# Kernel optimization log

Measured on AMD Instinct MI355X. Metric: run time of the kernel, lower is better.

The kernel has to match this reference:

```python
import jax, jax.numpy as jnp
import numpy as np

N_VISIBLE = 4096
N_HIDDEN = 4096
BATCH = 8192


def setup_inputs() -> dict:
    key = jax.random.key(0)
    k_x, k_w = jax.random.split(key)
    input_data = jax.random.uniform(k_x, (BATCH, N_VISIBLE), dtype=jnp.float32)
    # xavier_uniform with sigmoid gain (=1.0): limit = sqrt(6/(fan_in+fan_out))
    limit = float(np.sqrt(6.0 / (N_VISIBLE + N_HIDDEN)))
    W = jax.random.uniform(k_w, (N_VISIBLE, N_HIDDEN), dtype=jnp.float32,
                           minval=-limit, maxval=limit)
    hidden_bias = jnp.zeros((N_HIDDEN,), dtype=jnp.float32)
    return {"input_data": input_data, "W": W, "hidden_bias": hidden_bias}


def reference(input_data, W, hidden_bias):
    # RBM.sample_hidden_2 (forward): sigmoid(x @ W + b), batched over samples.
    # (The torch code loops per sample with host syncs; same math, vectorized.)
    hid_prob = jax.nn.sigmoid(jnp.matmul(input_data, W) + hidden_bias)
    return hid_prob
```

## Files before the change

kernel.cpp:

```cpp
#include <hip/hip_runtime.h>
#include <cstdint>

#define MDIM 8192
#define NDIM 4096
#define KDIM 4096

typedef __bf16 bf16x8 __attribute__((ext_vector_type(8)));
typedef float f32x4 __attribute__((ext_vector_type(4)));

__device__ __forceinline__ void gload_lds16(const void* g, void* l) {
    __builtin_amdgcn_global_load_lds(
        (const __attribute__((address_space(1))) uint32_t*)g,
        (__attribute__((address_space(3))) uint32_t*)l, 16, 0, 0);
}

__device__ __forceinline__ unsigned short bf16_bits(float f) {
    __bf16 b = (__bf16)f;
    return __builtin_bit_cast(unsigned short, b);
}

__device__ __forceinline__ int detect_f32(const void* X) {
    int ok = 1;
    if (threadIdx.x < 128) {
        unsigned short h = ((const unsigned short*)X)[threadIdx.x];
        ok = (h <= 0x3F80);
    }
    return __syncthreads_and(ok) ? 0 : 1;
}

__global__ __launch_bounds__(256) void cvt_x(const float* __restrict__ X,
                                             __bf16* __restrict__ Xb) {
    const int f32 = detect_f32(X);
    if (!f32) return;
    const long base = ((long)blockIdx.x * 256 + threadIdx.x) * 16;
#pragma unroll
    for (int c = 0; c < 2; ++c) {
        float4 v0 = *(const float4*)(X + base + c * 8);
        float4 v1 = *(const float4*)(X + base + c * 8 + 4);
        unsigned short r[8] = {bf16_bits(v0.x), bf16_bits(v0.y), bf16_bits(v0.z),
                               bf16_bits(v0.w), bf16_bits(v1.x), bf16_bits(v1.y),
                               bf16_bits(v1.z), bf16_bits(v1.w)};
        *(uint4*)(Xb + base + c * 8) = *(const uint4*)r;
    }
}

__global__ __launch_bounds__(256) void transpose_w(const void* __restrict__ X,
                                                   const void* __restrict__ W,
                                                   __bf16* __restrict__ WT) {
    __shared__ unsigned short tile[64 * 65];
    const int f32 = detect_f32(X);
    const int t = threadIdx.x;
    const int k0 = blockIdx.y * 64;
    const int n0 = blockIdx.x * 64;
    if (f32) {
        const float* Wf = (const float*)W;
#pragma unroll
        for (int p = 0; p < 4; ++p) {
            const int ch = p * 256 + t;
            const int kr = ch >> 4;
            const int nc = ch & 15;
            float4 v = *(const float4*)(Wf + (long)(k0 + kr) * NDIM + n0 + nc * 4);
            tile[(nc * 4 + 0) * 65 + kr] = bf16_bits(v.x);
            tile[(nc * 4 + 1) * 65 + kr] = bf16_bits(v.y);
            tile[(nc * 4 + 2) * 65 + kr] = bf16_bits(v.z);
            tile[(nc * 4 + 3) * 65 + kr] = bf16_bits(v.w);
        }
    } else {
        const __bf16* Wb = (const __bf16*)W;
#pragma unroll
        for (int p = 0; p < 2; ++p) {
            const int ch = p * 256 + t;
            const int kr = ch >> 3;
            const int nc = ch & 7;
            uint4 v = *(const uint4*)(Wb + (long)(k0 + kr) * NDIM + n0 + nc * 8);
            const unsigned short* e = (const unsigned short*)&v;
#pragma unroll
            for (int i = 0; i < 8; ++i) tile[(nc * 8 + i) * 65 + kr] = e[i];
        }
    }
    __syncthreads();
#pragma unroll
    for (int p = 0; p < 2; ++p) {
        const int ch = p * 256 + t;
        const int nr = ch >> 3;
        const int kc = ch & 7;
        unsigned short r[8];
#pragma unroll
        for (int i = 0; i < 8; ++i) r[i] = tile[nr * 65 + kc * 8 + i];
        *(uint4*)(WT + (long)(n0 + nr) * KDIM + k0 + kc * 8) = *(uint4*)r;
    }
}

template <int MODE>
__global__ __launch_bounds__(256) void gemm_bias_sigmoid(
    const void* __restrict__ X, const __bf16* __restrict__ Xb,
    const void* __restrict__ Wp, const __bf16* __restrict__ WT,
    const void* __restrict__ bias, void* __restrict__ out) {
    __shared__ __bf16 sA[128 * 32];
    __shared__ __bf16 sB[128 * 32];
    const int f32 = detect_f32(X);
    const int t = threadIdx.x;
    const int lane = t & 63;
    const int wid = t >> 6;
    const int m0 = blockIdx.y * 128;
    const int n0 = blockIdx.x * 128;
    const int wm = (wid & 1) * 64;
    const int wn = (wid >> 1) * 64;
    const int lrow = lane & 15;
    const int quad = lane >> 4;

    f32x4 acc[4][4] = {};

    const int srow = t >> 2;
    const int schk = t & 3;
    __bf16* ldsA = sA + wid * 512;
    __bf16* ldsB = sB + wid * 512;

    const int arow = t >> 1;
    const int acol = (t & 1) * 16;
    const int fp = t & 15;
    const int fc = t >> 4;
    uint32_t* sB32 = (uint32_t*)sB;

    auto compute = [&]() {
        bf16x8 aF[4], bF[4];
        const __bf16* pa = sA + (wm + lrow) * 32 + quad * 8;
        const __bf16* pb = sB + (wn + lrow) * 32 + quad * 8;
#pragma unroll
        for (int i = 0; i < 4; ++i) aF[i] = *(const bf16x8*)(pa + i * 512);
#pragma unroll
        for (int j = 0; j < 4; ++j) bF[j] = *(const bf16x8*)(pb + j * 512);
#pragma unroll
        for (int i = 0; i < 4; ++i)
#pragma unroll
            for (int j = 0; j < 4; ++j)
                acc[i][j] = __builtin_amdgcn_mfma_f32_16x16x32_bf16(
                    aF[i], bF[j], acc[i][j], 0, 0, 0);
    };

    if (MODE <= 1 && !(MODE == 1 && f32)) {
        const __bf16* Abf = (MODE == 0 && f32) ? Xb : (const __bf16*)X;
        const __bf16* gA = Abf + (long)(m0 + srow) * KDIM + schk * 8;
        const __bf16* gB = WT + (long)(n0 + srow) * KDIM + schk * 8;
        for (int kt = 0; kt < KDIM / 32; ++kt) {
            const __bf16* a0 = gA + kt * 32;
            gload_lds16(a0, ldsA);
            gload_lds16(a0 + (long)64 * KDIM, ldsA + 2048);
            const __bf16* b0 = gB + kt * 32;
            gload_lds16(b0, ldsB);
            gload_lds16(b0 + (long)64 * KDIM, ldsB + 2048);
            __syncthreads();
            compute();
            __syncthreads();
        }
    } else if (MODE == 1) {
        const float* Xf = (const float*)X;
        const __bf16* gB = WT + (long)(n0 + srow) * KDIM + schk * 8;
        for (int kt = 0; kt < KDIM / 32; ++kt) {
            const __bf16* b0 = gB + kt * 32;
            gload_lds16(b0, ldsB);
            gload_lds16(b0 + (long)64 * KDIM, ldsB + 2048);
            const float* ap = Xf + (long)(m0 + arow) * KDIM + kt * 32 + acol;
            float4 v0 = *(const float4*)(ap);
            float4 v1 = *(const float4*)(ap + 4);
            float4 v2 = *(const float4*)(ap + 8);
            float4 v3 = *(const float4*)(ap + 12);
            unsigned short r[16] = {
                bf16_bits(v0.x), bf16_bits(v0.y), bf16_bits(v0.z), bf16_bits(v0.w),
                bf16_bits(v1.x), bf16_bits(v1.y), bf16_bits(v1.z), bf16_bits(v1.w),
                bf16_bits(v2.x), bf16_bits(v2.y), bf16_bits(v2.z), bf16_bits(v2.w),
                bf16_bits(v3.x), bf16_bits(v3.y), bf16_bits(v3.z), bf16_bits(v3.w)};
            *(uint4*)(sA + arow * 32 + acol) = *(const uint4*)(r);
            *(uint4*)(sA + arow * 32 + acol + 8) = *(const uint4*)(r + 8);
            __syncthreads();
            compute();
            __syncthreads();
        }
    } else {
        if (!f32) {
            const __bf16* gA = (const __bf16*)X + (long)(m0 + srow) * KDIM + schk * 8;
            const __bf16* Wb = (const __bf16*)Wp;
            for (int kt = 0; kt < KDIM / 32; ++kt) {
                const __bf16* a0 = gA + kt * 32;
                gload_lds16(a0, ldsA);
                gload_lds16(a0 + (long)64 * KDIM, ldsA + 2048);
                const __bf16* w0 = Wb + (long)(kt * 32 + 2 * fp) * NDIM + n0 + fc * 8;
                uint4 g0 = *(const uint4*)(w0);
                uint4 g1 = *(const uint4*)(w0 + NDIM);
                const unsigned short* e0 = (const unsigned short*)&g0;
                const unsigned short* e1 = (const unsigned short*)&g1;
#pragma unroll
                for (int i = 0; i < 8; ++i)
                    sB32[(fc * 8 + i) * 16 + fp] =
                        (uint32_t)e0[i] | ((uint32_t)e1[i] << 16);
                __syncthreads();
                compute();
                __syncthreads();
            }
        } else {
            const float* Xf = (const float*)X;
            const float* Wf = (const float*)Wp;
            for (int kt = 0; kt < KDIM / 32; ++kt) {
                const float* ap = Xf + (long)(m0 + arow) * KDIM + kt * 32 + acol;
                float4 v0 = *(const float4*)(ap);
                float4 v1 = *(const float4*)(ap + 4);
                float4 v2 = *(const float4*)(ap + 8);
                float4 v3 = *(const float4*)(ap + 12);
                unsigned short r[16] = {
                    bf16_bits(v0.x), bf16_bits(v0.y), bf16_bits(v0.z), bf16_bits(v0.w),
                    bf16_bits(v1.x), bf16_bits(v1.y), bf16_bits(v1.z), bf16_bits(v1.w),
                    bf16_bits(v2.x), bf16_bits(v2.y), bf16_bits(v2.z), bf16_bits(v2.w),
                    bf16_bits(v3.x), bf16_bits(v3.y), bf16_bits(v3.z), bf16_bits(v3.w)};
                *(uint4*)(sA + arow * 32 + acol) = *(const uint4*)(r);
                *(uint4*)(sA + arow * 32 + acol + 8) = *(const uint4*)(r + 8);
                const float* w0 = Wf + (long)(kt * 32 + 2 * fp) * NDIM + n0 + fc * 8;
                float4 u0 = *(const float4*)(w0);
                float4 u1 = *(const float4*)(w0 + 4);
                float4 u2 = *(const float4*)(w0 + NDIM);
                float4 u3 = *(const float4*)(w0 + NDIM + 4);
                float k0v[8] = {u0.x, u0.y, u0.z, u0.w, u1.x, u1.y, u1.z, u1.w};
                float k1v[8] = {u2.x, u2.y, u2.z, u2.w, u3.x, u3.y, u3.z, u3.w};
#pragma unroll
                for (int i = 0; i < 8; ++i)
                    sB32[(fc * 8 + i) * 16 + fp] =
                        (uint32_t)bf16_bits(k0v[i]) |
                        ((uint32_t)bf16_bits(k1v[i]) << 16);
                __syncthreads();
                compute();
                __syncthreads();
            }
        }
    }

    const int crow = m0 + wm + quad * 4;
    if (f32) {
        float* of = (float*)out;
        const float* bf = (const float*)bias;
#pragma unroll
        for (int j = 0; j < 4; ++j) {
            const int col = n0 + wn + j * 16 + lrow;
            const float bv = bf[col];
#pragma unroll
            for (int i = 0; i < 4; ++i) {
                const long rbase = (long)(crow + i * 16) * NDIM + col;
#pragma unroll
                for (int r = 0; r < 4; ++r) {
                    const float x = acc[i][j][r] + bv;
                    of[rbase + (long)r * NDIM] = 1.0f / (1.0f + __expf(-x));
                }
            }
        }
    } else {
        __bf16* ob = (__bf16*)out;
        const __bf16* bb = (const __bf16*)bias;
#pragma unroll
        for (int j = 0; j < 4; ++j) {
            const int col = n0 + wn + j * 16 + lrow;
            const float bv = (float)bb[col];
#pragma unroll
            for (int i = 0; i < 4; ++i) {
                const long rbase = (long)(crow + i * 16) * NDIM + col;
#pragma unroll
                for (int r = 0; r < 4; ++r) {
                    const float x = acc[i][j][r] + bv;
                    ob[rbase + (long)r * NDIM] = (__bf16)(1.0f / (1.0f + __expf(-x)));
                }
            }
        }
    }
}

extern "C" void kernel_launch(void* const* d_in, const int* in_sizes, int n_in,
                              void* d_out, int out_size, void* d_ws,
                              size_t ws_size, hipStream_t stream) {
    const void* X = d_in[0];
    const void* W = d_in[1];
    const void* bias = d_in[2];

    const size_t wt_bytes = (size_t)KDIM * NDIM * sizeof(__bf16);
    const size_t xb_bytes = (size_t)MDIM * KDIM * sizeof(__bf16);
    dim3 gg(NDIM / 128, MDIM / 128);

    if (ws_size >= wt_bytes + xb_bytes) {
        __bf16* WT = (__bf16*)d_ws;
        __bf16* Xb = (__bf16*)((char*)d_ws + wt_bytes);
        cvt_x<<<MDIM * KDIM / (256 * 16), 256, 0, stream>>>((const float*)X, Xb);
        transpose_w<<<dim3(NDIM / 64, KDIM / 64), 256, 0, stream>>>(X, W, WT);
        gemm_bias_sigmoid<0><<<gg, 256, 0, stream>>>(X, Xb, W, WT, bias, d_out);
    } else if (ws_size >= wt_bytes) {
        __bf16* WT = (__bf16*)d_ws;
        transpose_w<<<dim3(NDIM / 64, KDIM / 64), 256, 0, stream>>>(X, W, WT);
        gemm_bias_sigmoid<1><<<gg, 256, 0, stream>>>(X, nullptr, W, WT, bias, d_out);
    } else {
        gemm_bias_sigmoid<2><<<gg, 256, 0, stream>>>(X, nullptr, W, nullptr, bias, d_out);
    }
}
```

Baseline: 628.2 us.

## Merge prep kernels into one launch and double GEMM K-tile to 64

Folds the X conversion and W transpose into a single prep kernel launch, indexed by block id, to save one launch. In MODE 0 the main GEMM now stages 64-wide K tiles (twice the LDS), so each barrier pair covers two MFMA sub-steps and the number of synchronisations halves. The cost is more LDS per block, which may lower occupancy. The LDS rows stay unswizzled at a 128-byte stride, so fragment reads may hit bank conflicts.

```diff
diff --git a/kernel.cpp b/kernel.cpp
--- a/kernel.cpp
+++ b/kernel.cpp
@@ -28,19 +28,68 @@
     return __syncthreads_and(ok) ? 0 : 1;
 }
 
-__global__ __launch_bounds__(256) void cvt_x(const float* __restrict__ X,
-                                             __bf16* __restrict__ Xb) {
+__global__ __launch_bounds__(256) void prep(const void* __restrict__ X,
+                                            const void* __restrict__ W,
+                                            __bf16* __restrict__ Xb,
+                                            __bf16* __restrict__ WT) {
     const int f32 = detect_f32(X);
-    if (!f32) return;
-    const long base = ((long)blockIdx.x * 256 + threadIdx.x) * 16;
-#pragma unroll
-    for (int c = 0; c < 2; ++c) {
-        float4 v0 = *(const float4*)(X + base + c * 8);
-        float4 v1 = *(const float4*)(X + base + c * 8 + 4);
-        unsigned short r[8] = {bf16_bits(v0.x), bf16_bits(v0.y), bf16_bits(v0.z),
-                               bf16_bits(v0.w), bf16_bits(v1.x), bf16_bits(v1.y),
-                               bf16_bits(v1.z), bf16_bits(v1.w)};
-        *(uint4*)(Xb + base + c * 8) = *(const uint4*)r;
+    const int t = threadIdx.x;
+    if (blockIdx.x < 8192) {
+        if (!f32) return;
+        const float* Xf = (const float*)X;
+        const long base = ((long)blockIdx.x * 256 + t) * 16;
+#pragma unroll
+        for (int c = 0; c < 2; ++c) {
+            float4 v0 = *(const float4*)(Xf + base + c * 8);
+            float4 v1 = *(const float4*)(Xf + base + c * 8 + 4);
+            unsigned short r[8] = {bf16_bits(v0.x), bf16_bits(v0.y),
+                                   bf16_bits(v0.z), bf16_bits(v0.w),
+                                   bf16_bits(v1.x), bf16_bits(v1.y),
+                                   bf16_bits(v1.z), bf16_bits(v1.w)};
+            *(uint4*)(Xb + base + c * 8) = *(const uint4*)r;
+        }
+        return;
+    }
+    __shared__ unsigned short tile[64 * 65];
+    const int bid = blockIdx.x - 8192;
+    const int n0 = (bid & 63) * 64;
+    const int k0 = (bid >> 6) * 64;
+    if (f32) {
+        const float* Wf = (const float*)W;
+#pragma unroll
+        for (int p = 0; p < 4; ++p) {
+            const int ch = p * 256 + t;
+            const int kr = ch >> 4;
+            const int nc = ch & 15;
+            float4 v = *(const float4*)(Wf + (long)(k0 + kr) * NDIM + n0 + nc * 4);
+            tile[(nc * 4 + 0) * 65 + kr] = bf16_bits(v.x);
+            tile[(nc * 4 + 1) * 65 + kr] = bf16_bits(v.y);
+            tile[(nc * 4 + 2) * 65 + kr] = bf16_bits(v.z);
+            tile[(nc * 4 + 3) * 65 + kr] = bf16_bits(v.w);
+        }
+    } else {
+        const __bf16* Wb = (const __bf16*)W;
+#pragma unroll
+        for (int p = 0; p < 2; ++p) {
+            const int ch = p * 256 + t;
+            const int kr = ch >> 3;
+            const int nc = ch & 7;
+            uint4 v = *(const uint4*)(Wb + (long)(k0 + kr) * NDIM + n0 + nc * 8);
+            const unsigned short* e = (const unsigned short*)&v;
+#pragma unroll
+            for (int i = 0; i < 8; ++i) tile[(nc * 8 + i) * 65 + kr] = e[i];
+        }
+    }
+    __syncthreads();
+#pragma unroll
+    for (int p = 0; p < 2; ++p) {
+        const int ch = p * 256 + t;
+        const int nr = ch >> 3;
+        const int kc = ch & 7;
+        unsigned short r[8];
+#pragma unroll
+        for (int i = 0; i < 8; ++i) r[i] = tile[nr * 65 + kc * 8 + i];
+        *(uint4*)(WT + (long)(n0 + nr) * KDIM + k0 + kc * 8) = *(uint4*)r;
     }
 }
 
@@ -96,8 +145,8 @@
     const void* __restrict__ X, const __bf16* __restrict__ Xb,
     const void* __restrict__ Wp, const __bf16* __restrict__ WT,
     const void* __restrict__ bias, void* __restrict__ out) {
-    __shared__ __bf16 sA[128 * 32];
-    __shared__ __bf16 sB[128 * 32];
+    __shared__ __bf16 sA[128 * 64];
+    __shared__ __bf16 sB[128 * 64];
     const int f32 = detect_f32(X);
     const int t = threadIdx.x;
     const int lane = t & 63;
@@ -111,73 +160,108 @@
 
     f32x4 acc[4][4] = {};
 
-    const int srow = t >> 2;
-    const int schk = t & 3;
-    __bf16* ldsA = sA + wid * 512;
-    __bf16* ldsB = sB + wid * 512;
-
-    const int arow = t >> 1;
-    const int acol = (t & 1) * 16;
-    const int fp = t & 15;
-    const int fc = t >> 4;
-    uint32_t* sB32 = (uint32_t*)sB;
-
-    auto compute = [&]() {
-        bf16x8 aF[4], bF[4];
-        const __bf16* pa = sA + (wm + lrow) * 32 + quad * 8;
-        const __bf16* pb = sB + (wn + lrow) * 32 + quad * 8;
-#pragma unroll
-        for (int i = 0; i < 4; ++i) aF[i] = *(const bf16x8*)(pa + i * 512);
-#pragma unroll
-        for (int j = 0; j < 4; ++j) bF[j] = *(const bf16x8*)(pb + j * 512);
-#pragma unroll
-        for (int i = 0; i < 4; ++i)
-#pragma unroll
-            for (int j = 0; j < 4; ++j)
-                acc[i][j] = __builtin_amdgcn_mfma_f32_16x16x32_bf16(
-                    aF[i], bF[j], acc[i][j], 0, 0, 0);
-    };
-
-    if (MODE <= 1 && !(MODE == 1 && f32)) {
-        const __bf16* Abf = (MODE == 0 && f32) ? Xb : (const __bf16*)X;
-        const __bf16* gA = Abf + (long)(m0 + srow) * KDIM + schk * 8;
-        const __bf16* gB = WT + (long)(n0 + srow) * KDIM + schk * 8;
-        for (int kt = 0; kt < KDIM / 32; ++kt) {
-            const __bf16* a0 = gA + kt * 32;
-            gload_lds16(a0, ldsA);
-            gload_lds16(a0 + (long)64 * KDIM, ldsA + 2048);
-            const __bf16* b0 = gB + kt * 32;
-            gload_lds16(b0, ldsB);
-            gload_lds16(b0 + (long)64 * KDIM, ldsB + 2048);
+    if constexpr (MODE == 0) {
+        const __bf16* Abf = f32 ? Xb : (const __bf16*)X;
+        const int r8 = lane >> 3;
+        const int c8 = lane & 7;
+        const __bf16* gA = Abf + (long)(m0 + wid * 32 + r8) * KDIM + c8 * 8;
+        const __bf16* gB = WT + (long)(n0 + wid * 32 + r8) * KDIM + c8 * 8;
+        __bf16* lA = sA + wid * 32 * 64;
+        __bf16* lB = sB + wid * 32 * 64;
+
+        for (int kt = 0; kt < KDIM / 64; ++kt) {
+            const int kb = kt * 64;
+#pragma unroll
+            for (int i = 0; i < 4; ++i) {
+                gload_lds16(gA + kb + (long)i * 8 * KDIM, lA + i * 512);
+                gload_lds16(gB + kb + (long)i * 8 * KDIM, lB + i * 512);
+            }
             __syncthreads();
-            compute();
+#pragma unroll
+            for (int h = 0; h < 2; ++h) {
+                bf16x8 aF[4], bF[4];
+                const __bf16* pa = sA + (wm + lrow) * 64 + h * 32 + quad * 8;
+                const __bf16* pb = sB + (wn + lrow) * 64 + h * 32 + quad * 8;
+#pragma unroll
+                for (int i = 0; i < 4; ++i)
+                    aF[i] = *(const bf16x8*)(pa + i * 1024);
+#pragma unroll
+                for (int j = 0; j < 4; ++j)
+                    bF[j] = *(const bf16x8*)(pb + j * 1024);
+#pragma unroll
+                for (int i = 0; i < 4; ++i)
+#pragma unroll
+                    for (int j = 0; j < 4; ++j)
+                        acc[i][j] = __builtin_amdgcn_mfma_f32_16x16x32_bf16(
+                            aF[i], bF[j], acc[i][j], 0, 0, 0);
+            }
             __syncthreads();
         }
-    } else if (MODE == 1) {
-        const float* Xf = (const float*)X;
-        const __bf16* gB = WT + (long)(n0 + srow) * KDIM + schk * 8;
-        for (int kt = 0; kt < KDIM / 32; ++kt) {
-            const __bf16* b0 = gB + kt * 32;
-            gload_lds16(b0, ldsB);
-            gload_lds16(b0 + (long)64 * KDIM, ldsB + 2048);
-            const float* ap = Xf + (long)(m0 + arow) * KDIM + kt * 32 + acol;
-            float4 v0 = *(const float4*)(ap);
-            float4 v1 = *(const float4*)(ap + 4);
-            float4 v2 = *(const float4*)(ap + 8);
-            float4 v3 = *(const float4*)(ap + 12);
-            unsigned short r[16] = {
-                bf16_bits(v0.x), bf16_bits(v0.y), bf16_bits(v0.z), bf16_bits(v0.w),
-                bf16_bits(v1.x), bf16_bits(v1.y), bf16_bits(v1.z), bf16_bits(v1.w),
-                bf16_bits(v2.x), bf16_bits(v2.y), bf16_bits(v2.z), bf16_bits(v2.w),
-                bf16_bits(v3.x), bf16_bits(v3.y), bf16_bits(v3.z), bf16_bits(v3.w)};
-            *(uint4*)(sA + arow * 32 + acol) = *(const uint4*)(r);
-            *(uint4*)(sA + arow * 32 + acol + 8) = *(const uint4*)(r + 8);
-            __syncthreads();
-            compute();
-            __syncthreads();
-        }
-    } else {
-        if (!f32) {
+    } else {
+        const int srow = t >> 2;
+        const int schk = t & 3;
+        __bf16* ldsA = sA + wid * 512;
+        __bf16* ldsB = sB + wid * 512;
+        const int arow = t >> 1;
+        const int acol = (t & 1) * 16;
+        const int fp = t & 15;
+        const int fc = t >> 4;
+        uint32_t* sB32 = (uint32_t*)sB;
+
+        auto compute = [&]() {
+            bf16x8 aF[4], bF[4];
+            const __bf16* pa = sA + (wm + lrow) * 32 + quad * 8;
+            const __bf16* pb = sB + (wn + lrow) * 32 + quad * 8;
+#pragma unroll
+            for (int i = 0; i < 4; ++i) aF[i] = *(const bf16x8*)(pa + i * 512);
+#pragma unroll
+            for (int j = 0; j < 4; ++j) bF[j] = *(const bf16x8*)(pb + j * 512);
+#pragma unroll
+            for (int i = 0; i < 4; ++i)
+#pragma unroll
+                for (int j = 0; j < 4; ++j)
+                    acc[i][j] = __builtin_amdgcn_mfma_f32_16x16x32_bf16(
+                        aF[i], bF[j], acc[i][j], 0, 0, 0);
+        };
+
+        if (MODE == 1 && !f32) {
+            const __bf16* gA = (const __bf16*)X + (long)(m0 + srow) * KDIM + schk * 8;
+            const __bf16* gB = WT + (long)(n0 + srow) * KDIM + schk * 8;
+            for (int kt = 0; kt < KDIM / 32; ++kt) {
+                const __bf16* a0 = gA + kt * 32;
+                gload_lds16(a0, ldsA);
+                gload_lds16(a0 + (long)64 * KDIM, ldsA + 2048);
+                const __bf16* b0 = gB + kt * 32;
+                gload_lds16(b0, ldsB);
+                gload_lds16(b0 + (long)64 * KDIM, ldsB + 2048);
+                __syncthreads();
+                compute();
+                __syncthreads();
+            }
+        } else if (MODE == 1) {
+            const float* Xf = (const float*)X;
+            const __bf16* gB = WT + (long)(n0 + srow) * KDIM + schk * 8;
+            for (int kt = 0; kt < KDIM / 32; ++kt) {
+                const __bf16* b0 = gB + kt * 32;
+                gload_lds16(b0, ldsB);
+                gload_lds16(b0 + (long)64 * KDIM, ldsB + 2048);
+                const float* ap = Xf + (long)(m0 + arow) * KDIM + kt * 32 + acol;
+                float4 v0 = *(const float4*)(ap);
+                float4 v1 = *(const float4*)(ap + 4);
+                float4 v2 = *(const float4*)(ap + 8);
+                float4 v3 = *(const float4*)(ap + 12);
+                unsigned short r[16] = {
+                    bf16_bits(v0.x), bf16_bits(v0.y), bf16_bits(v0.z), bf16_bits(v0.w),
+                    bf16_bits(v1.x), bf16_bits(v1.y), bf16_bits(v1.z), bf16_bits(v1.w),
+                    bf16_bits(v2.x), bf16_bits(v2.y), bf16_bits(v2.z), bf16_bits(v2.w),
+                    bf16_bits(v3.x), bf16_bits(v3.y), bf16_bits(v3.z), bf16_bits(v3.w)};
+                *(uint4*)(sA + arow * 32 + acol) = *(const uint4*)(r);
+                *(uint4*)(sA + arow * 32 + acol + 8) = *(const uint4*)(r + 8);
+                __syncthreads();
+                compute();
+                __syncthreads();
+            }
+        } else if (MODE == 2 && !f32) {
             const __bf16* gA = (const __bf16*)X + (long)(m0 + srow) * KDIM + schk * 8;
             const __bf16* Wb = (const __bf16*)Wp;
             for (int kt = 0; kt < KDIM / 32; ++kt) {
@@ -197,7 +281,7 @@
                 compute();
                 __syncthreads();
             }
-        } else {
+        } else if (MODE == 2) {
             const float* Xf = (const float*)X;
             const float* Wf = (const float*)Wp;
             for (int kt = 0; kt < KDIM / 32; ++kt) {
@@ -284,8 +368,7 @@
     if (ws_size >= wt_bytes + xb_bytes) {
         __bf16* WT = (__bf16*)d_ws;
         __bf16* Xb = (__bf16*)((char*)d_ws + wt_bytes);
-        cvt_x<<<MDIM * KDIM / (256 * 16), 256, 0, stream>>>((const float*)X, Xb);
-        transpose_w<<<dim3(NDIM / 64, KDIM / 64), 256, 0, stream>>>(X, W, WT);
+        prep<<<8192 + 4096, 256, 0, stream>>>(X, W, Xb, WT);
         gemm_bias_sigmoid<0><<<gg, 256, 0, stream>>>(X, Xb, W, WT, bias, d_out);
     } else if (ws_size >= wt_bytes) {
         __bf16* WT = (__bf16*)d_ws;
```

Result: slower. 660.9 us (+5.2%).
